# Kernel tuning notes

Measured on AMD Instinct MI355X. Metric: run time of the kernel, lower is better.

The kernel has to match this reference:

```python
import jax, jax.numpy as jnp
import numpy as np

N_EMBD = 2048
NUM_GROUPS = 8
EXPERTS_PER_GROUP = 8
ROUTER_TEMPERATURE = 1.0
N_TOKENS = 16384


def setup_inputs() -> dict:
    key = jax.random.key(0)
    kx, kg, ke = jax.random.split(key, 3)
    x = jax.random.normal(kx, (N_TOKENS, N_EMBD), dtype=jnp.float32)
    # nn.Linear(in, out, bias=False) stores weight as [out, in]; kaiming-uniform-ish scale
    bound = 1.0 / np.sqrt(N_EMBD)
    group_gate_w = jax.random.uniform(kg, (NUM_GROUPS, N_EMBD), dtype=jnp.float32,
                                      minval=-bound, maxval=bound)
    expert_gate_w = jax.random.uniform(ke, (NUM_GROUPS * EXPERTS_PER_GROUP, N_EMBD),
                                       dtype=jnp.float32, minval=-bound, maxval=bound)
    return {"x": x, "group_gate_w": group_gate_w, "expert_gate_w": expert_gate_w}


def reference(x, group_gate_w, expert_gate_w):
    N = x.shape[0]
    G = NUM_GROUPS
    E_g = EXPERTS_PER_GROUP
    inv_temp = 1.0 / ROUTER_TEMPERATURE

    # Level 1: group routing
    group_logits = jnp.einsum('nd,gd->ng', x, group_gate_w)            # [N, G]
    group_probs = jax.nn.softmax(group_logits * inv_temp, axis=-1)     # [N, G]
    group_mask = group_probs >= (1.0 / G)                              # [N, G]

    # Level 2: expert routing within each group
    expert_logits = jnp.einsum('nd,ed->ne', x, expert_gate_w)          # [N, G*E_g]
    expert_logits = expert_logits.reshape(N, G, E_g)
    expert_probs = jax.nn.softmax(expert_logits * inv_temp, axis=-1)   # [N, G, E_g]
    expert_mask = expert_probs >= (1.0 / E_g)                          # [N, G, E_g]

    valid_mask_3d = group_mask[:, :, None] & expert_mask               # [N, G, E_g]
    selected_weights_3d = (group_probs[:, :, None] * expert_probs) * valid_mask_3d.astype(x.dtype)

    valid_mask = valid_mask_3d.reshape(N, G * E_g)
    selected_weights = selected_weights_3d.reshape(N, G * E_g)
    weight_sum = jnp.clip(jnp.sum(selected_weights, axis=-1, keepdims=True), 1e-9, None)
    normalized_weights = selected_weights / weight_sum
    return (valid_mask, normalized_weights)
```

## Files before the change

kernel.cpp:

```cpp
#include <hip/hip_runtime.h>
#include <hip/hip_bf16.h>


#define NT 16384
#define NE 2048
#define KC 128
#define NCHUNK 16

#define QS    272
#define PL    1088
#define FP    2208
#define XB    44160
#define BUFSZ 79488
#define LDS_BYTES 158976

typedef _Float16 v8h __attribute__((ext_vector_type(8)));
typedef float    v4f __attribute__((ext_vector_type(4)));

__global__ __launch_bounds__(512, 2)
void router(const float* __restrict__ x, const float* __restrict__ gw,
            const float* __restrict__ ew, float* __restrict__ out)
{
    __shared__ __align__(16) char sm[LDS_BYTES];
    const int tid  = threadIdx.x;
    const int lane = tid & 63;
    const int w    = tid >> 6;
    const int t0   = blockIdx.x * 64;

    const float* wsrc[3]; int who[3]; int wmode[3];
    #pragma unroll
    for (int i = 0; i < 3; ++i) {
        int s = tid + i * 512;
        if (s >= 1280) { wmode[i] = 0; wsrc[i] = ew; who[i] = 0; continue; }
        int gate = s >> 4, kslot = s & 15;
        int ks = kslot >> 2, q = kslot & 3;
        who[i] = ((gate >> 4) * 4 + ks) * FP + q * QS + (gate & 15) * 16;
        if (gate < 64)      { wmode[i] = 2; wsrc[i] = ew + (size_t)gate * NE + kslot * 8; }
        else if (gate < 72) { wmode[i] = 2; wsrc[i] = gw + (size_t)(gate - 64) * NE + kslot * 8; }
        else                { wmode[i] = 1; wsrc[i] = ew; }
    }
    const float* xsrc[2]; int xho[2];
    #pragma unroll
    for (int i = 0; i < 2; ++i) {
        int s = tid + i * 512;
        int token = s >> 4, kslot = s & 15;
        int ks = kslot >> 2, q = kslot & 3;
        xho[i] = XB + ((token >> 4) * 4 + ks) * FP + q * QS + (token & 15) * 16;
        xsrc[i] = x + (size_t)(t0 + token) * NE + kslot * 8;
    }

    float4 wr[3][2], xr[2][2];

    auto stage_load = [&](int c) {
        const int kc = c * KC;
        #pragma unroll
        for (int i = 0; i < 3; ++i) {
            if (wmode[i] == 2) {
                wr[i][0] = *(const float4*)(wsrc[i] + kc);
                wr[i][1] = *(const float4*)(wsrc[i] + kc + 4);
            } else {
                wr[i][0] = make_float4(0.f, 0.f, 0.f, 0.f);
                wr[i][1] = make_float4(0.f, 0.f, 0.f, 0.f);
            }
        }
        #pragma unroll
        for (int i = 0; i < 2; ++i) {
            xr[i][0] = *(const float4*)(xsrc[i] + kc);
            xr[i][1] = *(const float4*)(xsrc[i] + kc + 4);
        }
    };

    auto split8 = [](const float4& a, const float4& b, v8h& h, v8h& l) {
        float v[8] = {a.x, a.y, a.z, a.w, b.x, b.y, b.z, b.w};
        #pragma unroll
        for (int j = 0; j < 8; ++j) {
            _Float16 hh = (_Float16)v[j];
            h[j] = hh;
            l[j] = (_Float16)((v[j] - (float)hh) * 2048.0f);
        }
    };

    auto stage_commit = [&](int buf) {
        const int bb = buf * BUFSZ;
        #pragma unroll
        for (int i = 0; i < 3; ++i) {
            if (wmode[i] == 0) continue;
            v8h h, l;
            split8(wr[i][0], wr[i][1], h, l);
            *(v8h*)(sm + bb + who[i])      = h;
            *(v8h*)(sm + bb + who[i] + PL) = l;
        }
        #pragma unroll
        for (int i = 0; i < 2; ++i) {
            v8h h, l;
            split8(xr[i][0], xr[i][1], h, l);
            *(v8h*)(sm + bb + xho[i])      = h;
            *(v8h*)(sm + bb + xho[i] + PL) = l;
        }
    };

    const int tt = w & 3, s2 = w >> 2;
    v4f accHH[5], accC[5];
    #pragma unroll
    for (int g = 0; g < 5; ++g) { accHH[g] = (v4f)(0.f); accC[g] = (v4f)(0.f); }
    const int rdo = (lane >> 4) * QS + (lane & 15) * 16;

    stage_load(0);
    stage_commit(0);
    for (int c = 0; c < NCHUNK; ++c) {
        if (c + 1 < NCHUNK) stage_load(c + 1);
        __syncthreads();
        {
            const int bb = (c & 1) * BUFSZ;
            #pragma unroll
            for (int ksl = 0; ksl < 2; ++ksl) {
                const int ks = s2 * 2 + ksl;
                const char* xb = sm + bb + XB + (tt * 4 + ks) * FP + rdo;
                v8h Bh = *(const v8h*)xb;
                v8h Bl = *(const v8h*)(xb + PL);
                #pragma unroll
                for (int g = 0; g < 5; ++g) {
                    const char* wb = sm + bb + (g * 4 + ks) * FP + rdo;
                    v8h Ah = *(const v8h*)wb;
                    v8h Al = *(const v8h*)(wb + PL);
                    accHH[g] = __builtin_amdgcn_mfma_f32_16x16x32_f16(Ah, Bh, accHH[g], 0, 0, 0);
                    accC[g]  = __builtin_amdgcn_mfma_f32_16x16x32_f16(Ah, Bl, accC[g], 0, 0, 0);
                    accC[g]  = __builtin_amdgcn_mfma_f32_16x16x32_f16(Al, Bh, accC[g], 0, 0, 0);
                }
            }
        }
        if (c + 1 < NCHUNK) stage_commit((c + 1) & 1);
    }
    __syncthreads();

    float part[5][4];
    #pragma unroll
    for (int g = 0; g < 5; ++g)
        #pragma unroll
        for (int r = 0; r < 4; ++r)
            part[g][r] = accHH[g][r] + accC[g][r] * (1.0f / 2048.0f);

    float* red = (float*)sm;
    if (w >= 4) {
        #pragma unroll
        for (int g = 0; g < 5; ++g)
            #pragma unroll
            for (int r = 0; r < 4; ++r)
                red[((tt * 5 + g) * 4 + r) * 64 + lane] = part[g][r];
    }
    __syncthreads();
    float* la = (float*)(sm + 24576);
    if (w < 4) {
        #pragma unroll
        for (int g = 0; g < 5; ++g)
            #pragma unroll
            for (int r = 0; r < 4; ++r) {
                float v = part[g][r] + red[((tt * 5 + g) * 4 + r) * 64 + lane];
                int gate  = g * 16 + (lane >> 4) * 4 + r;
                int token = tt * 16 + (lane & 15);
                la[token * 80 + gate] = v;
            }
    }
    __syncthreads();

    if (tid < 64) {
        const float* lg = la + tid * 80;
        float* M = (float*)(sm + 45056) + tid * 64;
        float* W = (float*)(sm + 61440) + tid * 64;

        float gpb[8];
        float gmax = lg[64];
        #pragma unroll
        for (int g = 1; g < 8; ++g) gmax = fmaxf(gmax, lg[64 + g]);
        float gsum = 0.f;
        #pragma unroll
        for (int g = 0; g < 8; ++g) { gpb[g] = __expf(lg[64 + g] - gmax); gsum += gpb[g]; }
        const float ginv = 1.f / gsum;

        float sel[64];
        float wsum = 0.f;
        #pragma unroll
        for (int g = 0; g < 8; ++g) {
            const float gp_ = gpb[g] * ginv;
            float emax = lg[g * 8];
            #pragma unroll
            for (int j = 1; j < 8; ++j) emax = fmaxf(emax, lg[g * 8 + j]);
            float ep[8]; float esum = 0.f;
            #pragma unroll
            for (int j = 0; j < 8; ++j) { ep[j] = __expf(lg[g * 8 + j] - emax); esum += ep[j]; }
            const float einv = 1.f / esum;
            const bool gm = gp_ >= 0.125f;
            #pragma unroll
            for (int j = 0; j < 8; ++j) {
                const float pe = ep[j] * einv;
                const bool v = gm && (pe >= 0.125f);
                const float ww = v ? gp_ * pe : 0.f;
                M[g * 8 + j] = v ? 1.f : 0.f;
                sel[g * 8 + j] = ww;
                wsum += ww;
            }
        }
        const float inv = 1.f / fmaxf(wsum, 1e-9f);
        #pragma unroll
        for (int e = 0; e < 64; ++e) W[e] = sel[e] * inv;
    }
    __syncthreads();

    const float4* M4 = (const float4*)(sm + 45056);
    const float4* W4 = (const float4*)(sm + 61440);
    float4* o0 = (float4*)(out + (size_t)t0 * 64);
    float4* o1 = (float4*)(out + (size_t)NT * 64 + (size_t)t0 * 64);
    o0[tid]       = M4[tid];
    o0[tid + 512] = M4[tid + 512];
    o1[tid]       = W4[tid];
    o1[tid + 512] = W4[tid + 512];
}

extern "C" void kernel_launch(void* const* d_in, const int* in_sizes, int n_in,
                              void* d_out, int out_size, void* d_ws, size_t ws_size,
                              hipStream_t stream) {
    const float* x  = (const float*)d_in[0];
    const float* gw = (const float*)d_in[1];
    const float* ew = (const float*)d_in[2];
    float* out = (float*)d_out;
    (void)d_ws; (void)ws_size;

    router<<<dim3(NT / 64), dim3(512), 0, stream>>>(x, gw, ew, out);
}
```

Measured before the change: 201.0 us.

## Pre-split gate weights in a prep kernel and shrink router tiles for occupancy

Adds a prep kernel that converts the gate weights once into fp16 hi/lo pairs laid out to match the router's shared-memory format. The router then copies these straight into LDS instead of re-splitting the weights in every block. The router now handles 32 tokens per block with a 32-wide K chunk, so LDS use is much smaller and the launch bound asks for 4 blocks per CU instead of 2. The catch is twice as many blocks, so the weight data is streamed more often in total, plus one extra kernel launch and a workspace buffer.

```diff
diff --git a/kernel.cpp b/kernel.cpp
--- a/kernel.cpp
+++ b/kernel.cpp
@@ -4,106 +4,122 @@
 
 #define NT 16384
 #define NE 2048
-#define KC 128
-#define NCHUNK 16
-
-#define QS    272
-#define PL    1088
-#define FP    2208
-#define XB    44160
-#define BUFSZ 79488
-#define LDS_BYTES 158976
+#define NCHUNK 32
+
+#define QS 272
+#define PL 1088
+#define FP 2208
+#define XB 22080
+#define BUFSZ 30912
+#define LDS_BYTES 61824
 
 typedef _Float16 v8h __attribute__((ext_vector_type(8)));
 typedef float    v4f __attribute__((ext_vector_type(4)));
 
-__global__ __launch_bounds__(512, 2)
-void router(const float* __restrict__ x, const float* __restrict__ gw,
-            const float* __restrict__ ew, float* __restrict__ out)
+__global__ __launch_bounds__(256)
+void prep(const float* __restrict__ gw, const float* __restrict__ ew,
+          float* __restrict__ Wbuf)
+{
+    const int u = blockIdx.x * 256 + threadIdx.x;
+    const int g4 = u >> 12, gk = (u >> 6) & 63, q = (u >> 4) & 3, gr = u & 15;
+    const int gate = g4 * 16 + gr;
+    const int k = gk * 32 + q * 8;
+    float v[8];
+    if (gate < 64) {
+        float4 a = *(const float4*)(ew + (size_t)gate * NE + k);
+        float4 b = *(const float4*)(ew + (size_t)gate * NE + k + 4);
+        v[0]=a.x; v[1]=a.y; v[2]=a.z; v[3]=a.w; v[4]=b.x; v[5]=b.y; v[6]=b.z; v[7]=b.w;
+    } else if (gate < 72) {
+        float4 a = *(const float4*)(gw + (size_t)(gate - 64) * NE + k);
+        float4 b = *(const float4*)(gw + (size_t)(gate - 64) * NE + k + 4);
+        v[0]=a.x; v[1]=a.y; v[2]=a.z; v[3]=a.w; v[4]=b.x; v[5]=b.y; v[6]=b.z; v[7]=b.w;
+    } else {
+        #pragma unroll
+        for (int j = 0; j < 8; ++j) v[j] = 0.f;
+    }
+    v8h h, l;
+    #pragma unroll
+    for (int j = 0; j < 8; ++j) {
+        _Float16 hh = (_Float16)v[j];
+        h[j] = hh;
+        l[j] = (_Float16)((v[j] - (float)hh) * 2048.0f);
+    }
+    char* p = (char*)Wbuf + (size_t)u * 32;
+    *(v8h*)p        = h;
+    *(v8h*)(p + 16) = l;
+}
+
+__global__ __launch_bounds__(512, 4)
+void router(const float* __restrict__ x, const float* __restrict__ Wbuf,
+            float* __restrict__ out)
 {
     __shared__ __align__(16) char sm[LDS_BYTES];
     const int tid  = threadIdx.x;
     const int lane = tid & 63;
     const int w    = tid >> 6;
-    const int t0   = blockIdx.x * 64;
-
-    const float* wsrc[3]; int who[3]; int wmode[3];
-    #pragma unroll
-    for (int i = 0; i < 3; ++i) {
-        int s = tid + i * 512;
-        if (s >= 1280) { wmode[i] = 0; wsrc[i] = ew; who[i] = 0; continue; }
-        int gate = s >> 4, kslot = s & 15;
-        int ks = kslot >> 2, q = kslot & 3;
-        who[i] = ((gate >> 4) * 4 + ks) * FP + q * QS + (gate & 15) * 16;
-        if (gate < 64)      { wmode[i] = 2; wsrc[i] = ew + (size_t)gate * NE + kslot * 8; }
-        else if (gate < 72) { wmode[i] = 2; wsrc[i] = gw + (size_t)(gate - 64) * NE + kslot * 8; }
-        else                { wmode[i] = 1; wsrc[i] = ew; }
-    }
-    const float* xsrc[2]; int xho[2];
-    #pragma unroll
-    for (int i = 0; i < 2; ++i) {
-        int s = tid + i * 512;
-        int token = s >> 4, kslot = s & 15;
-        int ks = kslot >> 2, q = kslot & 3;
-        xho[i] = XB + ((token >> 4) * 4 + ks) * FP + q * QS + (token & 15) * 16;
-        xsrc[i] = x + (size_t)(t0 + token) * NE + kslot * 8;
-    }
-
-    float4 wr[3][2], xr[2][2];
-
+    const int t0   = blockIdx.x * 32;
+
+    const char* w0src; int who0;
+    {
+        int g4 = tid >> 7, lks = (tid >> 6) & 1, q = (tid >> 4) & 3, gr = tid & 15;
+        w0src = (const char*)Wbuf + (size_t)((((g4*64 + lks)*4 + q)*16 + gr) * 32);
+        who0  = (g4*2 + lks)*FP + q*QS + gr*16;
+    }
+    const bool s1W = (tid < 128), s1X = (tid >= 128 && tid < 384);
+    const char* w1src = nullptr; int who1 = 0;
+    const float* xsrc = nullptr; int xho = 0;
+    if (s1W) {
+        int s = tid + 512;
+        int g4 = s >> 7, lks = (s >> 6) & 1, q = (s >> 4) & 3, gr = s & 15;
+        w1src = (const char*)Wbuf + (size_t)((((g4*64 + lks)*4 + q)*16 + gr) * 32);
+        who1  = (g4*2 + lks)*FP + q*QS + gr*16;
+    } else if (s1X) {
+        int i2 = tid - 128;
+        int q = i2 & 3, tr = (i2 >> 2) & 15, lks = (i2 >> 6) & 1, tt = (i2 >> 7) & 1;
+        xsrc = x + (size_t)(t0 + tt*16 + tr) * NE + lks*32 + q*8;
+        xho  = XB + (tt*2 + lks)*FP + q*QS + tr*16;
+    }
+
+    float4 wh0, wl0, wh1, wl1, xa, xb;
     auto stage_load = [&](int c) {
-        const int kc = c * KC;
-        #pragma unroll
-        for (int i = 0; i < 3; ++i) {
-            if (wmode[i] == 2) {
-                wr[i][0] = *(const float4*)(wsrc[i] + kc);
-                wr[i][1] = *(const float4*)(wsrc[i] + kc + 4);
-            } else {
-                wr[i][0] = make_float4(0.f, 0.f, 0.f, 0.f);
-                wr[i][1] = make_float4(0.f, 0.f, 0.f, 0.f);
-            }
-        }
-        #pragma unroll
-        for (int i = 0; i < 2; ++i) {
-            xr[i][0] = *(const float4*)(xsrc[i] + kc);
-            xr[i][1] = *(const float4*)(xsrc[i] + kc + 4);
+        const char* p0 = w0src + c * 4096;
+        wh0 = *(const float4*)p0;  wl0 = *(const float4*)(p0 + 16);
+        if (s1W) {
+            const char* p1 = w1src + c * 4096;
+            wh1 = *(const float4*)p1;  wl1 = *(const float4*)(p1 + 16);
+        } else if (s1X) {
+            xa = *(const float4*)(xsrc + c * 64);
+            xb = *(const float4*)(xsrc + c * 64 + 4);
         }
     };
-
-    auto split8 = [](const float4& a, const float4& b, v8h& h, v8h& l) {
-        float v[8] = {a.x, a.y, a.z, a.w, b.x, b.y, b.z, b.w};
-        #pragma unroll
-        for (int j = 0; j < 8; ++j) {
-            _Float16 hh = (_Float16)v[j];
-            h[j] = hh;
-            l[j] = (_Float16)((v[j] - (float)hh) * 2048.0f);
-        }
-    };
-
     auto stage_commit = [&](int buf) {
         const int bb = buf * BUFSZ;
-        #pragma unroll
-        for (int i = 0; i < 3; ++i) {
-            if (wmode[i] == 0) continue;
+        *(float4*)(sm + bb + who0)      = wh0;
+        *(float4*)(sm + bb + who0 + PL) = wl0;
+        if (s1W) {
+            *(float4*)(sm + bb + who1)      = wh1;
+            *(float4*)(sm + bb + who1 + PL) = wl1;
+        } else if (s1X) {
+            float v[8] = {xa.x, xa.y, xa.z, xa.w, xb.x, xb.y, xb.z, xb.w};
             v8h h, l;
-            split8(wr[i][0], wr[i][1], h, l);
-            *(v8h*)(sm + bb + who[i])      = h;
-            *(v8h*)(sm + bb + who[i] + PL) = l;
-        }
-        #pragma unroll
-        for (int i = 0; i < 2; ++i) {
-            v8h h, l;
-            split8(xr[i][0], xr[i][1], h, l);
-            *(v8h*)(sm + bb + xho[i])      = h;
-            *(v8h*)(sm + bb + xho[i] + PL) = l;
+            #pragma unroll
+            for (int j = 0; j < 8; ++j) {
+                _Float16 hh = (_Float16)v[j];
+                h[j] = hh;
+                l[j] = (_Float16)((v[j] - (float)hh) * 2048.0f);
+            }
+            *(v8h*)(sm + bb + xho)      = h;
+            *(v8h*)(sm + bb + xho + PL) = l;
         }
     };
 
-    const int tt = w & 3, s2 = w >> 2;
-    v4f accHH[5], accC[5];
+    const int tt = w & 1, s2 = (w >> 1) & 1, gh = w >> 2;
+    const int ng = gh ? 2 : 3, gbase = gh ? 3 : 0;
+    const int rdo = (lane >> 4) * QS + (lane & 15) * 16;
+
+    v4f accHH[3], accC[3];
     #pragma unroll
-    for (int g = 0; g < 5; ++g) { accHH[g] = (v4f)(0.f); accC[g] = (v4f)(0.f); }
-    const int rdo = (lane >> 4) * QS + (lane & 15) * 16;
+    for (int g = 0; g < 3; ++g) { accHH[g] = (v4f)(0.f); accC[g] = (v4f)(0.f); }
 
     stage_load(0);
     stage_commit(0);
@@ -112,61 +128,60 @@
         __syncthreads();
         {
             const int bb = (c & 1) * BUFSZ;
-            #pragma unroll
-            for (int ksl = 0; ksl < 2; ++ksl) {
-                const int ks = s2 * 2 + ksl;
-                const char* xb = sm + bb + XB + (tt * 4 + ks) * FP + rdo;
-                v8h Bh = *(const v8h*)xb;
-                v8h Bl = *(const v8h*)(xb + PL);
-                #pragma unroll
-                for (int g = 0; g < 5; ++g) {
-                    const char* wb = sm + bb + (g * 4 + ks) * FP + rdo;
-                    v8h Ah = *(const v8h*)wb;
-                    v8h Al = *(const v8h*)(wb + PL);
-                    accHH[g] = __builtin_amdgcn_mfma_f32_16x16x32_f16(Ah, Bh, accHH[g], 0, 0, 0);
-                    accC[g]  = __builtin_amdgcn_mfma_f32_16x16x32_f16(Ah, Bl, accC[g], 0, 0, 0);
-                    accC[g]  = __builtin_amdgcn_mfma_f32_16x16x32_f16(Al, Bh, accC[g], 0, 0, 0);
+            const char* xbp = sm + bb + XB + (tt*2 + s2)*FP + rdo;
+            v8h Bh = *(const v8h*)xbp;
+            v8h Bl = *(const v8h*)(xbp + PL);
+            #pragma unroll
+            for (int gi = 0; gi < 3; ++gi) {
+                if (gi < ng) {
+                    const char* wbp = sm + bb + ((gbase + gi)*2 + s2)*FP + rdo;
+                    v8h Ah = *(const v8h*)wbp;
+                    v8h Al = *(const v8h*)(wbp + PL);
+                    accHH[gi] = __builtin_amdgcn_mfma_f32_16x16x32_f16(Ah, Bh, accHH[gi], 0, 0, 0);
+                    accC[gi]  = __builtin_amdgcn_mfma_f32_16x16x32_f16(Ah, Bl, accC[gi], 0, 0, 0);
+                    accC[gi]  = __builtin_amdgcn_mfma_f32_16x16x32_f16(Al, Bh, accC[gi], 0, 0, 0);
                 }
             }
         }
         if (c + 1 < NCHUNK) stage_commit((c + 1) & 1);
     }
+
+    float part[3][4];
+    #pragma unroll
+    for (int gi = 0; gi < 3; ++gi)
+        #pragma unroll
+        for (int r = 0; r < 4; ++r)
+            part[gi][r] = accHH[gi][r] + accC[gi][r] * (1.0f / 2048.0f);
+
+    float* red = (float*)sm;
+    if (s2 == 1) {
+        #pragma unroll
+        for (int gi = 0; gi < 3; ++gi)
+            if (gi < ng)
+                #pragma unroll
+                for (int r = 0; r < 4; ++r)
+                    red[((tt*5 + gbase + gi)*4 + r)*64 + lane] = part[gi][r];
+    }
     __syncthreads();
-
-    float part[5][4];
-    #pragma unroll
-    for (int g = 0; g < 5; ++g)
-        #pragma unroll
-        for (int r = 0; r < 4; ++r)
-            part[g][r] = accHH[g][r] + accC[g][r] * (1.0f / 2048.0f);
-
-    float* red = (float*)sm;
-    if (w >= 4) {
-        #pragma unroll
-        for (int g = 0; g < 5; ++g)
-            #pragma unroll
-            for (int r = 0; r < 4; ++r)
-                red[((tt * 5 + g) * 4 + r) * 64 + lane] = part[g][r];
+    float* la = (float*)(sm + 12288);
+    if (s2 == 0) {
+        #pragma unroll
+        for (int gi = 0; gi < 3; ++gi)
+            if (gi < ng)
+                #pragma unroll
+                for (int r = 0; r < 4; ++r) {
+                    float v = part[gi][r] + red[((tt*5 + gbase + gi)*4 + r)*64 + lane];
+                    int gate  = (gbase + gi)*16 + (lane >> 4)*4 + r;
+                    int token = tt*16 + (lane & 15);
+                    la[token*80 + gate] = v;
+                }
     }
     __syncthreads();
-    float* la = (float*)(sm + 24576);
-    if (w < 4) {
-        #pragma unroll
-        for (int g = 0; g < 5; ++g)
-            #pragma unroll
-            for (int r = 0; r < 4; ++r) {
-                float v = part[g][r] + red[((tt * 5 + g) * 4 + r) * 64 + lane];
-                int gate  = g * 16 + (lane >> 4) * 4 + r;
-                int token = tt * 16 + (lane & 15);
-                la[token * 80 + gate] = v;
-            }
-    }
-    __syncthreads();
-
-    if (tid < 64) {
+
+    if (tid < 32) {
         const float* lg = la + tid * 80;
-        float* M = (float*)(sm + 45056) + tid * 64;
-        float* W = (float*)(sm + 61440) + tid * 64;
+        float* M = (float*)(sm + 24576) + tid * 64;
+        float* W = (float*)(sm + 32768) + tid * 64;
 
         float gpb[8];
         float gmax = lg[64];
@@ -206,14 +221,12 @@
     }
     __syncthreads();
 
-    const float4* M4 = (const float4*)(sm + 45056);
-    const float4* W4 = (const float4*)(sm + 61440);
+    const float4* M4 = (const float4*)(sm + 24576);
+    const float4* W4 = (const float4*)(sm + 32768);
     float4* o0 = (float4*)(out + (size_t)t0 * 64);
     float4* o1 = (float4*)(out + (size_t)NT * 64 + (size_t)t0 * 64);
-    o0[tid]       = M4[tid];
-    o0[tid + 512] = M4[tid + 512];
-    o1[tid]       = W4[tid];
-    o1[tid + 512] = W4[tid + 512];
+    o0[tid] = M4[tid];
+    o1[tid] = W4[tid];
 }
 
 extern "C" void kernel_launch(void* const* d_in, const int* in_sizes, int n_in,
@@ -222,8 +235,9 @@
     const float* x  = (const float*)d_in[0];
     const float* gw = (const float*)d_in[1];
     const float* ew = (const float*)d_in[2];
-    float* out = (float*)d_out;
-    (void)d_ws; (void)ws_size;
-
-    router<<<dim3(NT / 64), dim3(512), 0, stream>>>(x, gw, ew, out);
+    float* out  = (float*)d_out;
+    float* Wbuf = (float*)d_ws;
+
+    prep<<<dim3(80),  dim3(256), 0, stream>>>(gw, ew, Wbuf);
+    router<<<dim3(NT / 32), dim3(512), 0, stream>>>(x, Wbuf, out);
 }
```

New measurement: 231.9 us. 15.4% more time.
